# Kernel tuning notes

Measured on AMD Instinct MI355X. Metric: run time of the kernel, lower is better.

The kernel has to match this reference:

```python
import jax, jax.numpy as jnp
import numpy as np

B, S, D, H, L, FF, V, NB, G, C = 8, 1024, 256, 8, 2, 1024, 32000, 20000, 12, 4
DH = D // H


def _layer_norm(x, g, b, eps=1e-5):
    m = x.mean(-1, keepdims=True)
    v = ((x - m) ** 2).mean(-1, keepdims=True)
    return (x - m) / jnp.sqrt(v + eps) * g + b


def setup_inputs() -> dict:
    key = jax.random.key(0)
    ks = jax.random.split(key, 32)
    w = lambda k, shape, s=0.05: (jax.random.normal(k, shape, dtype=jnp.float32) * s)
    inp = {
        'input_ids': jax.random.randint(ks[0], (B, S), 0, V),
        'ngram_ids': jax.random.randint(ks[1], (V, G), 0, NB),
        'tfidf_scores': jax.random.uniform(ks[2], (V,), dtype=jnp.float32),
        'emb': jax.random.uniform(ks[3], (V, D), minval=-0.1, maxval=0.1, dtype=jnp.float32).at[0].set(0.0),  # padding_idx=0 row zeroed
        'pos_enc': jax.random.normal(ks[4], (1, S, D), dtype=jnp.float32) * 0.01,
        'bucket_emb': jax.random.uniform(ks[5], (NB, D), minval=-0.05, maxval=0.05, dtype=jnp.float32),
        'Wq': w(ks[6], (L, D, D)), 'bq': jnp.zeros((L, D)),
        'Wk': w(ks[7], (L, D, D)), 'bk': jnp.zeros((L, D)),
        'Wv': w(ks[8], (L, D, D)), 'bv': jnp.zeros((L, D)),
        'Wo': w(ks[9], (L, D, D)), 'bo': jnp.zeros((L, D)),
        'g1': jnp.ones((L, D)), 'be1': jnp.zeros((L, D)),
        'g2': jnp.ones((L, D)), 'be2': jnp.zeros((L, D)),
        'W1': w(ks[10], (L, D, FF)), 'b1': jnp.zeros((L, FF)),
        'W2': w(ks[11], (L, FF, D)), 'b2': jnp.zeros((L, D)),
        'alpha': jnp.full((L,), 0.1, dtype=jnp.float32),
        'gf': jnp.ones((D,)), 'bf': jnp.zeros((D,)),
        'Wc': jax.random.uniform(ks[12], (D, C), minval=-0.1, maxval=0.1, dtype=jnp.float32),
        'bc': jnp.zeros((C,)),
    }
    return inp


def reference(input_ids, ngram_ids, tfidf_scores, emb, pos_enc, bucket_emb,
              Wq, bq, Wk, bk, Wv, bv, Wo, bo, g1, be1, g2, be2,
              W1, b1, W2, b2, alpha, gf, bf, Wc, bc):
    pad_mask = input_ids == 0                      # (B,S) key padding mask
    x = emb[input_ids] + pos_enc[:, :S]            # (B,S,D)
    # char n-gram embedding: masked mean over n-gram buckets
    tok_ng = ngram_ids[jnp.clip(input_ids, 0, ngram_ids.shape[0] - 1)]   # (B,S,G)
    e_ng = bucket_emb[tok_ng]                       # (B,S,G,D)
    m = (tok_ng != 0)[..., None].astype(x.dtype)
    x = x + (e_ng * m).sum(axis=2) / jnp.clip(m.sum(axis=2), 1.0, None)
    # TF-IDF bias per key position
    bias_base = tfidf_scores[jnp.clip(input_ids, 0, tfidf_scores.shape[0] - 1)]  # (B,S)
    scale = DH ** -0.5
    for l in range(L):
        x2 = _layer_norm(x, g1[l], be1[l])
        Q = (x2 @ Wq[l] + bq[l]).reshape(B, S, H, DH).transpose(0, 2, 1, 3)
        K = (x2 @ Wk[l] + bk[l]).reshape(B, S, H, DH).transpose(0, 2, 1, 3)
        Vv = (x2 @ Wv[l] + bv[l]).reshape(B, S, H, DH).transpose(0, 2, 1, 3)
        scores = jnp.einsum('bhqd,bhkd->bhqk', Q, K) * scale
        scores = scores + (bias_base * alpha[l])[:, None, None, :]
        scores = jnp.where(pad_mask[:, None, None, :], -jnp.inf, scores)
        attn = jax.nn.softmax(scores, axis=-1)
        out = jnp.einsum('bhqk,bhkd->bhqd', attn, Vv).transpose(0, 2, 1, 3).reshape(B, S, D)
        x = x + (out @ Wo[l] + bo[l])
        x2 = _layer_norm(x, g2[l], be2[l])
        x = x + (jax.nn.relu(x2 @ W1[l] + b1[l]) @ W2[l] + b2[l])
    x = _layer_norm(x, gf, bf)
    return x[:, 0] @ Wc + bc                        # CLS pooling -> (B,4)
```

## Files before the change

kernel.cpp:

```cpp
#include <hip/hip_runtime.h>
#include <hip/hip_bf16.h>
#include <math.h>

#define TOK 8192
#define DIM 256
#define SEQ 1024
#define NH 8
#define FFD 1024
#define NL 2
#define VOCAB 32000
#define QKSTRIDE 2097152

typedef short bf16x8 __attribute__((ext_vector_type(8)));
typedef float f32x4 __attribute__((ext_vector_type(4)));

__device__ __forceinline__ ushort f2bf(float f) {
  union { float f; uint32_t u; } v; v.f = f;
  uint32_t r = v.u + 0x7FFFu + ((v.u >> 16) & 1u);
  return (ushort)(r >> 16);
}

__device__ __forceinline__ float bf2f(ushort u) {
  union { uint32_t u; float f; } v; v.u = (uint32_t)u << 16; return v.f;
}

__device__ __forceinline__ float exp2_n(float x) {
  float r; asm("v_exp_f32 %0, %1" : "=v"(r) : "v"(x)); return r;
}

__device__ __forceinline__ uint32_t cvtpk(float lo, float hi) {
  uint32_t r; asm("v_cvt_pk_bf16_f32 %0, %1, %2" : "=v"(r) : "v"(lo), "v"(hi));
  return r;
}

__device__ __forceinline__ void gload_lds16(const ushort* gp, ushort* lp) {
  __builtin_amdgcn_global_load_lds(
      (const __attribute__((address_space(1))) void*)gp,
      (__attribute__((address_space(3))) void*)lp, 16, 0, 0);
}

__global__ __launch_bounds__(256) void embed_ln_kernel(
    const int* __restrict__ ids, const int* __restrict__ ngram_ids,
    const float* __restrict__ tfidf, const float* __restrict__ emb,
    const float* __restrict__ pos, const float* __restrict__ bucket,
    const float* __restrict__ alpha, const float* __restrict__ g1,
    const float* __restrict__ be1,
    float* __restrict__ x, ushort* __restrict__ x2b, float* __restrict__ bm2)
{
  __shared__ int ngs[4][12];
  const int wave = threadIdx.x >> 6, lane = threadIdx.x & 63;
  const int t = blockIdx.x * 4 + wave;
  const int id = ids[t];
  int idc = id; if (idc < 0) idc = 0; if (idc > VOCAB-1) idc = VOCAB-1;
  if (lane < 12) ngs[wave][lane] = ngram_ids[idc*12 + lane];
  if (lane == 0) {
    const float tf = tfidf[idc];
    const bool msk = (id == 0);
    const float l2e = 1.4426950408889634f;
    bm2[t]       = msk ? -1e30f : tf * alpha[0] * l2e;
    bm2[TOK + t] = msk ? -1e30f : tf * alpha[1] * l2e;
  }
  __syncthreads();
  const int d0 = lane * 4;
  const int s = t & (SEQ - 1);
  float4 v = *reinterpret_cast<const float4*>(emb + (size_t)id*DIM + d0);
  const float4 p4 = *reinterpret_cast<const float4*>(pos + s*DIM + d0);
  v.x += p4.x; v.y += p4.y; v.z += p4.z; v.w += p4.w;
  float4 sum = {0.f, 0.f, 0.f, 0.f}; int cnt = 0;
  #pragma unroll
  for (int g = 0; g < 12; ++g) {
    const int ng = ngs[wave][g];
    if (ng != 0) {
      const float4 b4 = *reinterpret_cast<const float4*>(bucket + (size_t)ng*DIM + d0);
      sum.x += b4.x; sum.y += b4.y; sum.z += b4.z; sum.w += b4.w;
      cnt++;
    }
  }
  const float inv = 1.f / fmaxf((float)cnt, 1.0f);
  v.x += sum.x*inv; v.y += sum.y*inv; v.z += sum.z*inv; v.w += sum.w*inv;
  *reinterpret_cast<float4*>(x + (size_t)t*DIM + d0) = v;
  float sm = v.x + v.y + v.z + v.w;
  #pragma unroll
  for (int o = 32; o >= 1; o >>= 1) sm += __shfl_xor(sm, o);
  const float mean = sm * (1.f/256.f);
  const float dx0 = v.x-mean, dx1 = v.y-mean, dx2 = v.z-mean, dx3 = v.w-mean;
  float q = dx0*dx0 + dx1*dx1 + dx2*dx2 + dx3*dx3;
  #pragma unroll
  for (int o = 32; o >= 1; o >>= 1) q += __shfl_xor(q, o);
  const float rs = rsqrtf(q * (1.f/256.f) + 1e-5f);
  const float4 gv = *reinterpret_cast<const float4*>(g1 + d0);
  const float4 bv = *reinterpret_cast<const float4*>(be1 + d0);
  ushort4 o4;
  o4.x = f2bf(dx0*rs*gv.x + bv.x);
  o4.y = f2bf(dx1*rs*gv.y + bv.y);
  o4.z = f2bf(dx2*rs*gv.z + bv.z);
  o4.w = f2bf(dx3*rs*gv.w + bv.w);
  *reinterpret_cast<ushort4*>(x2b + (size_t)t*DIM + d0) = o4;
}

__global__ __launch_bounds__(256) void ln_bf16(
    const float* __restrict__ x, const float* __restrict__ g,
    const float* __restrict__ b, ushort* __restrict__ y)
{
  const int wave = threadIdx.x >> 6, lane = threadIdx.x & 63;
  const int row = blockIdx.x * 4 + wave;
  const float* xr = x + (size_t)row * DIM;
  float4 v = *reinterpret_cast<const float4*>(xr + lane*4);
  float s = v.x + v.y + v.z + v.w;
  #pragma unroll
  for (int o = 32; o >= 1; o >>= 1) s += __shfl_xor(s, o);
  const float mean = s * (1.f/256.f);
  const float dx0 = v.x-mean, dx1 = v.y-mean, dx2 = v.z-mean, dx3 = v.w-mean;
  float q = dx0*dx0 + dx1*dx1 + dx2*dx2 + dx3*dx3;
  #pragma unroll
  for (int o = 32; o >= 1; o >>= 1) q += __shfl_xor(q, o);
  const float rs = rsqrtf(q * (1.f/256.f) + 1e-5f);
  float4 gv = *reinterpret_cast<const float4*>(g + lane*4);
  float4 bv = *reinterpret_cast<const float4*>(b + lane*4);
  ushort4 o4;
  o4.x = f2bf(dx0*rs*gv.x + bv.x);
  o4.y = f2bf(dx1*rs*gv.y + bv.y);
  o4.z = f2bf(dx2*rs*gv.z + bv.z);
  o4.w = f2bf(dx3*rs*gv.w + bv.w);
  *reinterpret_cast<ushort4*>(y + (size_t)row*DIM + lane*4) = o4;
}

struct TDesc { const float* src; ushort* dst; int K; int N; };
struct TDescs { TDesc d[12]; };

__global__ __launch_bounds__(256) void transpose_conv(TDescs descs)
{
  const TDesc t = descs.d[blockIdx.z];
  const int k0 = blockIdx.x * 32, n0 = blockIdx.y * 32;
  if (k0 >= t.K || n0 >= t.N) return;
  __shared__ float tile[32][33];
  const int r = threadIdx.x >> 5, cc = threadIdx.x & 31;
  #pragma unroll
  for (int i = 0; i < 4; ++i)
    tile[r + i*8][cc] = t.src[(size_t)(k0 + r + i*8)*t.N + n0 + cc];
  __syncthreads();
  #pragma unroll
  for (int i = 0; i < 4; ++i)
    t.dst[(size_t)(n0 + r + i*8)*t.K + k0 + cc] = f2bf(tile[cc][r + i*8]);
}

template<int KDIM, int NDIM, int MODE>
__global__ __launch_bounds__(256) void gemm_mfma(
    const ushort* __restrict__ A, const ushort* __restrict__ Bw,
    const float* __restrict__ bias0, const float* __restrict__ bias1,
    const float* __restrict__ bias2, void* __restrict__ Cout,
    ushort* __restrict__ vtb)
{
  __shared__ ushort Al[3][64*32];
  __shared__ ushort Bl[3][128*32];
  const int bm = blockIdx.y * 64, bn = blockIdx.x * 128;
  const int tid = threadIdx.x, w = tid >> 6, lane = tid & 63;
  const int g = lane >> 4, c = lane & 15;
  const int lrow = lane >> 2, lc8 = (lane & 3) << 3;
  const f32x4 fzero = {0.f, 0.f, 0.f, 0.f};
  f32x4 acc[4][2];
  #pragma unroll
  for (int m = 0; m < 4; ++m) { acc[m][0] = fzero; acc[m][1] = fzero; }

#define STAGE(buf, k0)                                                         \
  {                                                                            \
    _Pragma("unroll")                                                          \
    for (int ch = w; ch < 12; ch += 4) {                                       \
      if (ch < 4)                                                              \
        gload_lds16(A + (size_t)(bm + ch*16 + lrow)*KDIM + (k0) + lc8,         \
                    &Al[buf][ch*512]);                                         \
      else                                                                     \
        gload_lds16(Bw + (size_t)(bn + (ch-4)*16 + lrow)*KDIM + (k0) + lc8,    \
                    &Bl[buf][(ch-4)*512]);                                     \
    }                                                                          \
  }

#define COMPUTE(buf)                                                           \
  {                                                                            \
    bf16x8 af[4], bfr[2];                                                      \
    _Pragma("unroll")                                                          \
    for (int m = 0; m < 4; ++m)                                                \
      af[m] = *(const bf16x8*)&Al[buf][(m*16 + c)*32 + g*8];                   \
    _Pragma("unroll")                                                          \
    for (int n = 0; n < 2; ++n)                                                \
      bfr[n] = *(const bf16x8*)&Bl[buf][(w*32 + n*16 + c)*32 + g*8];           \
    _Pragma("unroll")                                                          \
    for (int m = 0; m < 4; ++m)                                                \
      _Pragma("unroll")                                                        \
      for (int n = 0; n < 2; ++n)                                              \
        acc[m][n] = __builtin_amdgcn_mfma_f32_16x16x32_bf16(af[m], bfr[n], acc[m][n], 0, 0, 0); \
  }

  STAGE(0, 0);
  STAGE(1, 32);
  STAGE(2, 64);
  int buf = 0;
  for (int k0 = 0; k0 + 64 < KDIM; k0 += 32) {
    asm volatile("s_waitcnt vmcnt(6)" ::: "memory");
    __builtin_amdgcn_s_barrier();
    COMPUTE(buf);
    asm volatile("s_waitcnt lgkmcnt(0)" ::: "memory");
    __builtin_amdgcn_s_barrier();
    if (k0 + 96 < KDIM) STAGE(buf, k0 + 96);
    buf = (buf == 2) ? 0 : buf + 1;
  }
  asm volatile("s_waitcnt vmcnt(3)" ::: "memory");
  __builtin_amdgcn_s_barrier();
  COMPUTE(buf);
  buf = (buf == 2) ? 0 : buf + 1;
  asm volatile("s_waitcnt vmcnt(0)" ::: "memory");
  __builtin_amdgcn_s_barrier();
  COMPUTE(buf);
#undef STAGE
#undef COMPUTE

  #pragma unroll
  for (int m = 0; m < 4; ++m) {
    const int row0 = bm + m*16 + g*4;
    #pragma unroll
    for (int n = 0; n < 2; ++n) {
      const int col = bn + w*32 + n*16 + c;
      if (MODE == 1) {
        const float bb = bias0[col];
        #pragma unroll
        for (int r = 0; r < 4; ++r) {
          const float vv = fmaxf(acc[m][n][r] + bb, 0.f);
          const float other = __shfl_xor(vv, 1);
          if ((c & 1) == 0) {
            const uint32_t word = (uint32_t)f2bf(vv) | ((uint32_t)f2bf(other) << 16);
            *(uint32_t*)((ushort*)Cout + (size_t)(row0 + r)*NDIM + col) = word;
          }
        }
      } else if (MODE == 4) {
        const int b_ = row0 >> 10, s = row0 & (SEQ - 1);
        const int hd = col & 255;
        const int hh = hd >> 5, d = hd & 31;
        const float bb = (col < 256) ? bias0[hd] : bias1[hd];
        ushort* dst = ((col < 256) ? (ushort*)Cout : vtb)
                    + (((size_t)(b_*NH + hh)*SEQ + s) << 5) + d;
        #pragma unroll
        for (int r = 0; r < 4; ++r) {
          const float vv = acc[m][n][r] + bb;
          const float other = __shfl_xor(vv, 1);
          if ((c & 1) == 0) {
            const uint32_t word = (uint32_t)f2bf(vv) | ((uint32_t)f2bf(other) << 16);
            *(uint32_t*)(dst + (r << 5)) = word;
          }
        }
      } else {
        const int b_ = row0 >> 10, s = row0 & (SEQ - 1);
        if (col < 512) {
          const int hd = col & 255;
          const int hh = hd >> 5, d = hd & 31;
          const float bb = (col < 256) ? bias0[hd] : bias1[hd];
          ushort* dst = (ushort*)Cout + (col < 256 ? 0 : QKSTRIDE)
                      + (((size_t)(b_*NH + hh)*SEQ + s) << 5) + d;
          #pragma unroll
          for (int r = 0; r < 4; ++r) {
            const float vv = acc[m][n][r] + bb;
            const float other = __shfl_xor(vv, 1);
            if ((c & 1) == 0) {
              const uint32_t word = (uint32_t)f2bf(vv) | ((uint32_t)f2bf(other) << 16);
              *(uint32_t*)(dst + (r << 5)) = word;
            }
          }
        } else {
          const int hd = col - 512;
          const int hh = hd >> 5, d = hd & 31;
          const float bb = bias2[hd];
          const int sg = s >> 5, a = (s & 31) >> 2;
          const int pbase = (a & 3)*8 + (a >> 2)*4;
          ushort4 w4;
          w4.x = f2bf(acc[m][n][0] + bb);
          w4.y = f2bf(acc[m][n][1] + bb);
          w4.z = f2bf(acc[m][n][2] + bb);
          w4.w = f2bf(acc[m][n][3] + bb);
          *(ushort4*)(vtb + (((size_t)((b_*NH + hh)*32 + sg)*32 + d) << 5) + pbase) = w4;
        }
      }
    }
  }
}

template<int KDIM>
__global__ __launch_bounds__(256) void gemm64_acc(
    const ushort* __restrict__ A, const ushort* __restrict__ Bw,
    const float* __restrict__ bias, float* __restrict__ C)
{
  __shared__ ushort Al[3][64*32];
  __shared__ ushort Bl[3][64*32];
  const int bm = blockIdx.y * 64, bn = blockIdx.x * 64;
  const int tid = threadIdx.x, w = tid >> 6, lane = tid & 63;
  const int wm = w >> 1, wn = w & 1;
  const int g = lane >> 4, c = lane & 15;
  const int lrow = tid >> 2, lc8 = (tid & 3) << 3;
  const f32x4 fzero = {0.f, 0.f, 0.f, 0.f};
  f32x4 acc[2][2];
  acc[0][0] = fzero; acc[0][1] = fzero; acc[1][0] = fzero; acc[1][1] = fzero;

#define STAGE64(buf, k0)                                                       \
  {                                                                            \
    gload_lds16(A  + (size_t)(bm + lrow)*KDIM + (k0) + lc8,                    \
                &Al[buf][lrow*32 + lc8]);                                      \
    gload_lds16(Bw + (size_t)(bn + lrow)*KDIM + (k0) + lc8,                    \
                &Bl[buf][lrow*32 + lc8]);                                      \
  }

#define COMPUTE64(buf)                                                         \
  {                                                                            \
    bf16x8 af[2], bfr[2];                                                      \
    _Pragma("unroll")                                                          \
    for (int m = 0; m < 2; ++m)                                                \
      af[m] = *(const bf16x8*)&Al[buf][(wm*32 + m*16 + c)*32 + g*8];           \
    _Pragma("unroll")                                                          \
    for (int n = 0; n < 2; ++n)                                                \
      bfr[n] = *(const bf16x8*)&Bl[buf][(wn*32 + n*16 + c)*32 + g*8];          \
    _Pragma("unroll")                                                          \
    for (int m = 0; m < 2; ++m)                                                \
      _Pragma("unroll")                                                        \
      for (int n = 0; n < 2; ++n)                                              \
        acc[m][n] = __builtin_amdgcn_mfma_f32_16x16x32_bf16(af[m], bfr[n], acc[m][n], 0, 0, 0); \
  }

  STAGE64(0, 0);
  STAGE64(1, 32);
  STAGE64(2, 64);
  int buf = 0;
  for (int k0 = 0; k0 + 64 < KDIM; k0 += 32) {
    asm volatile("s_waitcnt vmcnt(4)" ::: "memory");
    __builtin_amdgcn_s_barrier();
    COMPUTE64(buf);
    asm volatile("s_waitcnt lgkmcnt(0)" ::: "memory");
    __builtin_amdgcn_s_barrier();
    if (k0 + 96 < KDIM) STAGE64(buf, k0 + 96);
    buf = (buf == 2) ? 0 : buf + 1;
  }
  asm volatile("s_waitcnt vmcnt(2)" ::: "memory");
  __builtin_amdgcn_s_barrier();
  COMPUTE64(buf);
  buf = (buf == 2) ? 0 : buf + 1;
  asm volatile("s_waitcnt vmcnt(0)" ::: "memory");
  __builtin_amdgcn_s_barrier();
  COMPUTE64(buf);
#undef STAGE64
#undef COMPUTE64

  #pragma unroll
  for (int m = 0; m < 2; ++m) {
    const int row0 = bm + wm*32 + m*16 + g*4;
    #pragma unroll
    for (int n = 0; n < 2; ++n) {
      const int col = bn + wn*32 + n*16 + c;
      const float bb = bias[col];
      #pragma unroll
      for (int r = 0; r < 4; ++r)
        C[(size_t)(row0 + r)*DIM + col] += acc[m][n][r] + bb;
    }
  }
}

__global__ __launch_bounds__(256) void attn_mfma(
    const ushort* __restrict__ qh, const ushort* __restrict__ kh,
    const ushort* __restrict__ vph, const float* __restrict__ bm2l,
    ushort* __restrict__ O)
{
  const int bid = blockIdx.x;
  const int lin = ((bid & 7) << 8) + (bid >> 3);
  const int tid = threadIdx.x, w = tid >> 6, lane = tid & 63;
  const int qw = lin & 31, h = (lin >> 5) & 7, b = lin >> 8;
  const int qb = qw << 5;
  const float scale2 = 0.17677669529663687f * 1.4426950408889634f;
  const int g = lane >> 4, c = lane & 15;
  const f32x4 fzero = {0.f, 0.f, 0.f, 0.f};
  const size_t bh = (size_t)(b*NH + h);

  const bf16x8 qf0 = *(const bf16x8*)(qh + ((bh*SEQ + qb + c)      << 5) + g*8);
  const bf16x8 qf1 = *(const bf16x8*)(qh + ((bh*SEQ + qb + 16 + c) << 5) + g*8);
  const ushort* kbase = kh  + ((bh*SEQ) << 5) + g*8;
  const ushort* vbase = vph + ((bh*SEQ) << 5) + g*8;
  const float*  bmb   = bm2l + b*SEQ;

  f32x4 oacc[2][2];
  oacc[0][0] = fzero; oacc[0][1] = fzero; oacc[1][0] = fzero; oacc[1][1] = fzero;
  float l0 = 0.f, l1 = 0.f;

  bf16x8 kfA[4], kfB[4];
  bf16x8 vfA[2][2], vfB[2][2];

#define LOADT(kt, kf, vf)                                                      \
  {                                                                            \
    _Pragma("unroll")                                                          \
    for (int ks = 0; ks < 4; ++ks)                                             \
      kf[ks] = *(const bf16x8*)(kbase + (((kt) + ks*16 + c) << 5));            \
    _Pragma("unroll")                                                          \
    for (int ds_ = 0; ds_ < 2; ++ds_)                                          \
      _Pragma("unroll")                                                        \
      for (int sg = 0; sg < 2; ++sg)                                           \
        vf[ds_][sg] = *(const bf16x8*)(vbase +                                 \
            (((((kt) >> 5) + sg)*32 + ds_*16 + c) << 5));                      \
  }

#define ATILE(kf, vf, kt)                                                      \
  {                                                                            \
    f32x4 sf0[4], sf1[4];                                                      \
    __builtin_amdgcn_s_setprio(1);                                             \
    _Pragma("unroll")                                                          \
    for (int ks = 0; ks < 4; ++ks)                                             \
      sf0[ks] = __builtin_amdgcn_mfma_f32_16x16x32_bf16(kf[ks], qf0, fzero, 0, 0, 0); \
    _Pragma("unroll")                                                          \
    for (int ks = 0; ks < 4; ++ks)                                             \
      sf1[ks] = __builtin_amdgcn_mfma_f32_16x16x32_bf16(kf[ks], qf1, fzero, 0, 0, 0); \
    __builtin_amdgcn_s_setprio(0);                                             \
    float e0[4][4], e1[4][4];                                                  \
    _Pragma("unroll")                                                          \
    for (int ks = 0; ks < 4; ++ks) {                                           \
      const f32x4 bb = *(const f32x4*)(bmb + (kt) + ks*16 + g*4);              \
      _Pragma("unroll")                                                        \
      for (int r = 0; r < 4; ++r) {                                            \
        e0[ks][r] = exp2_n(fmaf(sf0[ks][r], scale2, bb[r]));                   \
        e1[ks][r] = exp2_n(fmaf(sf1[ks][r], scale2, bb[r]));                   \
      }                                                                        \
    }                                                                          \
    float a0 = 0.f, a1 = 0.f, a2 = 0.f, a3 = 0.f;                              \
    _Pragma("unroll")                                                          \
    for (int r = 0; r < 4; ++r) {                                              \
      a0 += e0[0][r] + e0[1][r]; a1 += e0[2][r] + e0[3][r];                    \
      a2 += e1[0][r] + e1[1][r]; a3 += e1[2][r] + e1[3][r];                    \
    }                                                                          \
    l0 += a0 + a1; l1 += a2 + a3;                                              \
    union { bf16x8 v; uint32_t u[4]; } p00, p01, p10, p11;                     \
    p00.u[0] = cvtpk(e0[0][0], e0[0][1]); p00.u[1] = cvtpk(e0[0][2], e0[0][3]);\
    p00.u[2] = cvtpk(e0[1][0], e0[1][1]); p00.u[3] = cvtpk(e0[1][2], e0[1][3]);\
    p01.u[0] = cvtpk(e0[2][0], e0[2][1]); p01.u[1] = cvtpk(e0[2][2], e0[2][3]);\
    p01.u[2] = cvtpk(e0[3][0], e0[3][1]); p01.u[3] = cvtpk(e0[3][2], e0[3][3]);\
    p10.u[0] = cvtpk(e1[0][0], e1[0][1]); p10.u[1] = cvtpk(e1[0][2], e1[0][3]);\
    p10.u[2] = cvtpk(e1[1][0], e1[1][1]); p10.u[3] = cvtpk(e1[1][2], e1[1][3]);\
    p11.u[0] = cvtpk(e1[2][0], e1[2][1]); p11.u[1] = cvtpk(e1[2][2], e1[2][3]);\
    p11.u[2] = cvtpk(e1[3][0], e1[3][1]); p11.u[3] = cvtpk(e1[3][2], e1[3][3]);\
    __builtin_amdgcn_s_setprio(1);                                             \
    oacc[0][0] = __builtin_amdgcn_mfma_f32_16x16x32_bf16(vf[0][0], p00.v, oacc[0][0], 0, 0, 0); \
    oacc[0][1] = __builtin_amdgcn_mfma_f32_16x16x32_bf16(vf[1][0], p00.v, oacc[0][1], 0, 0, 0); \
    oacc[1][0] = __builtin_amdgcn_mfma_f32_16x16x32_bf16(vf[0][0], p10.v, oacc[1][0], 0, 0, 0); \
    oacc[1][1] = __builtin_amdgcn_mfma_f32_16x16x32_bf16(vf[1][0], p10.v, oacc[1][1], 0, 0, 0); \
    oacc[0][0] = __builtin_amdgcn_mfma_f32_16x16x32_bf16(vf[0][1], p01.v, oacc[0][0], 0, 0, 0); \
    oacc[0][1] = __builtin_amdgcn_mfma_f32_16x16x32_bf16(vf[1][1], p01.v, oacc[0][1], 0, 0, 0); \
    oacc[1][0] = __builtin_amdgcn_mfma_f32_16x16x32_bf16(vf[0][1], p11.v, oacc[1][0], 0, 0, 0); \
    oacc[1][1] = __builtin_amdgcn_mfma_f32_16x16x32_bf16(vf[1][1], p11.v, oacc[1][1], 0, 0, 0); \
    __builtin_amdgcn_s_setprio(0);                                             \
  }

  const int kt0 = w << 8;
  LOADT(kt0, kfA, vfA);
  LOADT(kt0 + 64, kfB, vfB);
  ATILE(kfA, vfA, kt0);
  LOADT(kt0 + 128, kfA, vfA);
  ATILE(kfB, vfB, kt0 + 64);
  LOADT(kt0 + 192, kfB, vfB);
  ATILE(kfA, vfA, kt0 + 128);
  ATILE(kfB, vfB, kt0 + 192);
#undef LOADT
#undef ATILE

  __shared__ float Lo[4][64][19];
  #pragma unroll
  for (int q = 0; q < 2; ++q)
    #pragma unroll
    for (int ds_ = 0; ds_ < 2; ++ds_)
      #pragma unroll
      for (int i = 0; i < 4; ++i)
        Lo[w][lane][q*8 + ds_*4 + i] = oacc[q][ds_][i];
  Lo[w][lane][16] = l0;
  Lo[w][lane][17] = l1;
  __syncthreads();
  if (w < 2) {
    const int q = w;
    float o[8] = {0.f,0.f,0.f,0.f,0.f,0.f,0.f,0.f};
    float ls = 0.f;
    #pragma unroll
    for (int ww = 0; ww < 4; ++ww) {
      ls += Lo[ww][lane][16 + q];
      #pragma unroll
      for (int i = 0; i < 8; ++i) o[i] += Lo[ww][lane][q*8 + i];
    }
    ls += __shfl_xor(ls, 16);
    ls += __shfl_xor(ls, 32);
    const float inv = 1.f / ls;
    ushort* orow = O + (size_t)(b*SEQ + qb + q*16 + c)*DIM + h*32 + g*4;
    const uint32_t w0 = (uint32_t)f2bf(o[0]*inv) | ((uint32_t)f2bf(o[1]*inv) << 16);
    const uint32_t w1 = (uint32_t)f2bf(o[2]*inv) | ((uint32_t)f2bf(o[3]*inv) << 16);
    const uint32_t w2 = (uint32_t)f2bf(o[4]*inv) | ((uint32_t)f2bf(o[5]*inv) << 16);
    const uint32_t w3 = (uint32_t)f2bf(o[6]*inv) | ((uint32_t)f2bf(o[7]*inv) << 16);
    *(uint32_t*)(orow)      = w0;
    *(uint32_t*)(orow + 2)  = w1;
    *(uint32_t*)(orow + 16) = w2;
    *(uint32_t*)(orow + 18) = w3;
  }
}

__global__ __launch_bounds__(256) void decode512(
    const ushort* __restrict__ x2b, const ushort* __restrict__ Wq1,
    const float* __restrict__ bq1, const ushort* __restrict__ kh,
    const ushort* __restrict__ vh, const float* __restrict__ bm2l,
    float* __restrict__ P)
{
  const int lin = blockIdx.x;
  const int ks = lin & 3, bh = lin >> 2;
  const int b = bh >> 3, h = bh & 7;
  const int tid = threadIdx.x;
  const float scale2 = 0.17677669529663687f * 1.4426950408889634f;
  __shared__ float xrow[256];
  __shared__ float qv[32];
  xrow[tid] = bf2f(x2b[(size_t)(b*SEQ)*DIM + tid]);
  __syncthreads();
  if (tid < 32) {
    const ushort* wrow = Wq1 + (size_t)(h*32 + tid)*DIM;
    float acc = bq1[h*32 + tid];
    #pragma unroll
    for (int k8 = 0; k8 < 32; ++k8) {
      const bf16x8 wv = *(const bf16x8*)(wrow + k8*8);
      #pragma unroll
      for (int j = 0; j < 8; ++j)
        acc = fmaf(bf2f((ushort)wv[j]), xrow[k8*8 + j], acc);
    }
    qv[tid] = acc;
  }
  __syncthreads();
  const int key = ks*256 + tid;
  const ushort* kr = kh + (((size_t)bh*SEQ + key) << 5);
  float dot = 0.f;
  #pragma unroll
  for (int i = 0; i < 4; ++i) {
    const bf16x8 kv8 = *(const bf16x8*)(kr + i*8);
    #pragma unroll
    for (int j = 0; j < 8; ++j)
      dot = fmaf(bf2f((ushort)kv8[j]), qv[i*8 + j], dot);
  }
  const float e = exp2_n(fmaf(dot, scale2, bm2l[b*SEQ + key]));
  const ushort* vr = vh + (((size_t)bh*SEQ + key) << 5);
  __shared__ float red[256][33];
  #pragma unroll
  for (int i = 0; i < 4; ++i) {
    const bf16x8 vv8 = *(const bf16x8*)(vr + i*8);
    #pragma unroll
    for (int j = 0; j < 8; ++j)
      red[tid][i*8 + j] = e * bf2f((ushort)vv8[j]);
  }
  red[tid][32] = e;
  __syncthreads();
  for (int s = 128; s >= 1; s >>= 1) {
    for (int i = tid; i < s*33; i += 256) {
      const int r = i / 33, d = i - r*33;
      red[r][d] += red[r + s][d];
    }
    __syncthreads();
  }
  if (tid < 33) P[((size_t)bh*4 + ks)*33 + tid] = red[0][tid];
}

__global__ __launch_bounds__(256) void wo_part(
    const float* __restrict__ P, const ushort* __restrict__ WoT1,
    const float* __restrict__ bo1, float* __restrict__ wo_out)
{
  const int cc = blockIdx.x, tid = threadIdx.x;
  __shared__ float orow[8][256];
  {
    const int b = tid >> 5, d32 = tid & 31;
    #pragma unroll
    for (int h = 0; h < 8; ++h) {
      const float* pp = P + ((size_t)(b*8 + h)*4)*33;
      float ov = 0.f, l = 0.f;
      #pragma unroll
      for (int ks = 0; ks < 4; ++ks) { ov += pp[ks*33 + d32]; l += pp[ks*33 + 32]; }
      orow[b][h*32 + d32] = ov / l;
    }
  }
  __syncthreads();
  const int w = tid >> 6, lane = tid & 63;
  const int col = cc*4 + w;
  const ushort* wrow = WoT1 + (size_t)col*DIM + lane*4;
  float wk[4];
  #pragma unroll
  for (int j = 0; j < 4; ++j) wk[j] = bf2f(wrow[j]);
  #pragma unroll
  for (int b = 0; b < 8; ++b) {
    float p = 0.f;
    #pragma unroll
    for (int j = 0; j < 4; ++j) p = fmaf(wk[j], orow[b][lane*4 + j], p);
    #pragma unroll
    for (int off = 32; off >= 1; off >>= 1) p += __shfl_xor(p, off);
    if (lane == 0) wo_out[b*DIM + col] = p + bo1[col];
  }
}

__global__ __launch_bounds__(256) void ff1_part(
    const float* __restrict__ x, const float* __restrict__ wo_out,
    const float* __restrict__ g21, const float* __restrict__ be21,
    const ushort* __restrict__ W1T1, const float* __restrict__ b11,
    float* __restrict__ mid)
{
  const int cc = blockIdx.x, tid = threadIdx.x;
  const int wave = tid >> 6, lane = tid & 63;
  __shared__ float trow[8][256];
  #pragma unroll
  for (int b = 0; b < 8; ++b)
    trow[b][tid] = x[(size_t)(b*SEQ)*DIM + tid] + wo_out[b*DIM + tid];
  __syncthreads();
  #pragma unroll
  for (int bb_ = 0; bb_ < 2; ++bb_) {
    const int b = wave + bb_*4;
    float4 vv = *(float4*)&trow[b][lane*4];
    float sm = vv.x + vv.y + vv.z + vv.w;
    #pragma unroll
    for (int o = 32; o >= 1; o >>= 1) sm += __shfl_xor(sm, o);
    const float mean = sm * (1.f/256.f);
    const float dx0 = vv.x-mean, dx1 = vv.y-mean, dx2 = vv.z-mean, dx3 = vv.w-mean;
    float q = dx0*dx0 + dx1*dx1 + dx2*dx2 + dx3*dx3;
    #pragma unroll
    for (int o = 32; o >= 1; o >>= 1) q += __shfl_xor(q, o);
    const float rs = rsqrtf(q * (1.f/256.f) + 1e-5f);
    const float4 gv = *(const float4*)(g21 + lane*4);
    const float4 bv = *(const float4*)(be21 + lane*4);
    float4 nv;
    nv.x = dx0*rs*gv.x + bv.x;
    nv.y = dx1*rs*gv.y + bv.y;
    nv.z = dx2*rs*gv.z + bv.z;
    nv.w = dx3*rs*gv.w + bv.w;
    *(float4*)&trow[b][lane*4] = nv;
  }
  __syncthreads();
  const int dotid = tid >> 1;
  const int col = cc*16 + (dotid & 15);
  const int b = dotid >> 4;
  const int kh_ = (tid & 1) * 128;
  const ushort* wrow = W1T1 + (size_t)col*DIM + kh_;
  float acc = 0.f;
  #pragma unroll
  for (int k8 = 0; k8 < 16; ++k8) {
    const bf16x8 wv = *(const bf16x8*)(wrow + k8*8);
    #pragma unroll
    for (int j = 0; j < 8; ++j)
      acc = fmaf(bf2f((ushort)wv[j]), trow[b][kh_ + k8*8 + j], acc);
  }
  acc += __shfl_xor(acc, 1);
  if ((tid & 1) == 0) mid[b*FFD + col] = fmaxf(acc + b11[col], 0.f);
}

__global__ __launch_bounds__(256) void ff2_part(
    const float* __restrict__ mid, const ushort* __restrict__ W2T1,
    const float* __restrict__ b21, const float* __restrict__ x,
    const float* __restrict__ wo_out, float* __restrict__ y2)
{
  const int cc = blockIdx.x, tid = threadIdx.x;
  __shared__ float mrow[8][1024];
  #pragma unroll
  for (int i = 0; i < 32; ++i) {
    const int idx = i*256 + tid;
    mrow[idx >> 10][idx & 1023] = mid[idx];
  }
  __syncthreads();
  const int dotid = tid >> 3;
  const int col = cc*4 + (dotid & 3);
  const int b = dotid >> 2;
  const int seg = (tid & 7) * 128;
  const ushort* wrow = W2T1 + (size_t)col*FFD + seg;
  float acc = 0.f;
  #pragma unroll
  for (int k8 = 0; k8 < 16; ++k8) {
    const bf16x8 wv = *(const bf16x8*)(wrow + k8*8);
    #pragma unroll
    for (int j = 0; j < 8; ++j)
      acc = fmaf(bf2f((ushort)wv[j]), mrow[b][seg + k8*8 + j], acc);
  }
  acc += __shfl_xor(acc, 1);
  acc += __shfl_xor(acc, 2);
  acc += __shfl_xor(acc, 4);
  if ((tid & 7) == 0)
    y2[b*DIM + col] = x[(size_t)(b*SEQ)*DIM + col] + wo_out[b*DIM + col]
                    + acc + b21[col];
}

__global__ __launch_bounds__(256) void cls2(
    const float* __restrict__ y2, const float* __restrict__ gf,
    const float* __restrict__ bfb, const float* __restrict__ Wc,
    const float* __restrict__ bc, float* __restrict__ out)
{
  const int b = blockIdx.x, tid = threadIdx.x;
  const int wave = tid >> 6, lane = tid & 63;
  const float v = y2[b*DIM + tid];
  __shared__ float redm[4], redv[4], redc[4][4];
  float s = v;
  #pragma unroll
  for (int o = 32; o >= 1; o >>= 1) s += __shfl_xor(s, o);
  if (lane == 0) redm[wave] = s;
  __syncthreads();
  const float mean = (redm[0]+redm[1]+redm[2]+redm[3]) * (1.f/256.f);
  const float dv = v - mean;
  float q = dv * dv;
  #pragma unroll
  for (int o = 32; o >= 1; o >>= 1) q += __shfl_xor(q, o);
  if (lane == 0) redv[wave] = q;
  __syncthreads();
  const float var = (redv[0]+redv[1]+redv[2]+redv[3]) * (1.f/256.f);
  const float rs = rsqrtf(var + 1e-5f);
  const float yn = dv*rs*gf[tid] + bfb[tid];
  float pc[4];
  #pragma unroll
  for (int cc = 0; cc < 4; ++cc) pc[cc] = yn * Wc[tid*4 + cc];
  #pragma unroll
  for (int cc = 0; cc < 4; ++cc) {
    #pragma unroll
    for (int o = 32; o >= 1; o >>= 1) pc[cc] += __shfl_xor(pc[cc], o);
  }
  if (lane == 0) {
    #pragma unroll
    for (int cc = 0; cc < 4; ++cc) redc[wave][cc] = pc[cc];
  }
  __syncthreads();
  if (tid < 4)
    out[b*4 + tid] = redc[0][tid] + redc[1][tid] + redc[2][tid] + redc[3][tid] + bc[tid];
}

extern "C" void kernel_launch(void* const* d_in, const int* in_sizes, int n_in,
                              void* d_out, int out_size, void* d_ws, size_t ws_size,
                              hipStream_t stream)
{
  const int*   ids    = (const int*)d_in[0];
  const int*   ngrams = (const int*)d_in[1];
  const float* tfidf  = (const float*)d_in[2];
  const float* emb    = (const float*)d_in[3];
  const float* pos    = (const float*)d_in[4];
  const float* bucket = (const float*)d_in[5];
  const float* Wq = (const float*)d_in[6];  const float* bq = (const float*)d_in[7];
  const float* Wk = (const float*)d_in[8];  const float* bk = (const float*)d_in[9];
  const float* Wv = (const float*)d_in[10]; const float* bv = (const float*)d_in[11];
  const float* Wo = (const float*)d_in[12]; const float* bo = (const float*)d_in[13];
  const float* g1 = (const float*)d_in[14]; const float* be1= (const float*)d_in[15];
  const float* g2 = (const float*)d_in[16]; const float* be2= (const float*)d_in[17];
  const float* W1 = (const float*)d_in[18]; const float* b1 = (const float*)d_in[19];
  const float* W2 = (const float*)d_in[20]; const float* b2 = (const float*)d_in[21];
  const float* alpha = (const float*)d_in[22];
  const float* gf = (const float*)d_in[23]; const float* bf = (const float*)d_in[24];
  const float* Wc = (const float*)d_in[25]; const float* bc = (const float*)d_in[26];

  uint8_t* base = (uint8_t*)d_ws;
  float*  x      = (float*)  base;
  ushort* x2b    = (ushort*)(base + 8388608);
  ushort* qkh    = (ushort*)(base + 12582912);
  ushort* vtb    = (ushort*)(base + 20971520);
  ushort* attb   = (ushort*)(base + 25165824);
  ushort* midb   = (ushort*)(base + 29360128);
  float*  bm2    = (float*) (base + 46137344);
  ushort* WqkvT  = (ushort*)(base + 46202880);
  ushort* WoT    = (ushort*)(base + 46989312);
  ushort* W1T    = (ushort*)(base + 47251456);
  ushort* W2T    = (ushort*)(base + 48300032);

  float* P       = (float*)(base + 25165824);
  float* wo_out  = (float*)(base + 25165824 + 65536);
  float* midf    = (float*)(base + 25165824 + 90112);
  float* y2      = (float*)(base + 25165824 + 122880);

  TDescs td;
  for (int l = 0; l < NL; ++l) {
    td.d[6*l+0] = { Wq + (size_t)l*DIM*DIM, WqkvT + (size_t)l*768*DIM +   0*DIM, DIM, DIM };
    td.d[6*l+1] = { Wk + (size_t)l*DIM*DIM, WqkvT + (size_t)l*768*DIM + 256*DIM, DIM, DIM };
    td.d[6*l+2] = { Wv + (size_t)l*DIM*DIM, WqkvT + (size_t)l*768*DIM + 512*DIM, DIM, DIM };
    td.d[6*l+3] = { Wo + (size_t)l*DIM*DIM, WoT  + (size_t)l*DIM*DIM,  DIM, DIM };
    td.d[6*l+4] = { W1 + (size_t)l*DIM*FFD, W1T  + (size_t)l*FFD*DIM,  DIM, FFD };
    td.d[6*l+5] = { W2 + (size_t)l*FFD*DIM, W2T  + (size_t)l*DIM*FFD,  FFD, DIM };
  }
  transpose_conv<<<dim3(32, 32, 12), 256, 0, stream>>>(td);

  embed_ln_kernel<<<TOK/4, 256, 0, stream>>>(
      ids, ngrams, tfidf, emb, pos, bucket, alpha, g1, be1, x, x2b, bm2);

  const dim3 gqkv(6, TOK/64), gkv(4, TOK/64), gff1(8, TOK/64), g64(4, TOK/64);

  gemm_mfma<256, 768, 3><<<gqkv, 256, 0, stream>>>(
      x2b, WqkvT, bq, bk, bv, qkh, vtb);
  attn_mfma<<<2048, 256, 0, stream>>>(qkh, qkh + QKSTRIDE, vtb, bm2, attb);
  gemm64_acc<256><<<g64, 256, 0, stream>>>(attb, WoT, bo, x);
  ln_bf16<<<TOK/4, 256, 0, stream>>>(x, g2, be2, x2b);
  gemm_mfma<256, 1024, 1><<<gff1, 256, 0, stream>>>(
      x2b, W1T, b1, nullptr, nullptr, midb, nullptr);
  gemm64_acc<1024><<<g64, 256, 0, stream>>>(midb, W2T, b2, x);

  ln_bf16<<<TOK/4, 256, 0, stream>>>(x, g1 + DIM, be1 + DIM, x2b);
  gemm_mfma<256, 512, 4><<<gkv, 256, 0, stream>>>(
      x2b, WqkvT + (size_t)768*DIM + 256*DIM, bk + DIM, bv + DIM, nullptr,
      qkh + QKSTRIDE, vtb);
  decode512<<<256, 256, 0, stream>>>(
      x2b, WqkvT + (size_t)768*DIM, bq + DIM,
      qkh + QKSTRIDE, vtb, bm2 + TOK, P);
  wo_part<<<64, 256, 0, stream>>>(P, WoT + DIM*DIM, bo + DIM, wo_out);
  ff1_part<<<64, 256, 0, stream>>>(x, wo_out, g2 + DIM, be2 + DIM,
                                   W1T + FFD*DIM, b1 + FFD, midf);
  ff2_part<<<64, 256, 0, stream>>>(midf, W2T + DIM*FFD, b2 + DIM, x, wo_out, y2);
  cls2<<<8, 256, 0, stream>>>(y2, gf, bf, Wc, bc, (float*)d_out);
}
```

Baseline: 143.7 us.

## Split attention warps across query and key groups, halving block count

The attention kernel now gives each block 64 queries instead of 32, with its four warps arranged as two query groups by two key halves of 512 keys each, in place of four key quarters over the same 32 queries. The grid shrinks from 2048 to 1024 blocks, and the cross-warp reduction now sums two partials per query group and writes both 16-row sub-tiles. This halves the block-level overhead and the reduction work per output row, at the cost of longer per-warp key loops and fewer blocks to spread across compute units.

```diff
diff --git a/kernel.cpp b/kernel.cpp
--- a/kernel.cpp
+++ b/kernel.cpp
@@ -365,10 +365,11 @@
     ushort* __restrict__ O)
 {
   const int bid = blockIdx.x;
-  const int lin = ((bid & 7) << 8) + (bid >> 3);
+  const int lin = ((bid & 7) << 7) + (bid >> 3);
   const int tid = threadIdx.x, w = tid >> 6, lane = tid & 63;
-  const int qw = lin & 31, h = (lin >> 5) & 7, b = lin >> 8;
-  const int qb = qw << 5;
+  const int q64 = lin & 15, h = (lin >> 4) & 7, b = lin >> 7;
+  const int qg = w >> 1, kg = w & 1;
+  const int qb = (q64 << 6) + (qg << 5);
   const float scale2 = 0.17677669529663687f * 1.4426950408889634f;
   const int g = lane >> 4, c = lane & 15;
   const f32x4 fzero = {0.f, 0.f, 0.f, 0.f};
@@ -449,15 +450,14 @@
     __builtin_amdgcn_s_setprio(0);                                             \
   }
 
-  const int kt0 = w << 8;
+  const int kt0 = kg << 9;
   LOADT(kt0, kfA, vfA);
-  LOADT(kt0 + 64, kfB, vfB);
-  ATILE(kfA, vfA, kt0);
-  LOADT(kt0 + 128, kfA, vfA);
-  ATILE(kfB, vfB, kt0 + 64);
-  LOADT(kt0 + 192, kfB, vfB);
-  ATILE(kfA, vfA, kt0 + 128);
-  ATILE(kfB, vfB, kt0 + 192);
+  for (int kt = kt0; kt < kt0 + 512; kt += 128) {
+    LOADT(kt + 64, kfB, vfB);
+    ATILE(kfA, vfA, kt);
+    if (kt + 128 < kt0 + 512) LOADT(kt + 128, kfA, vfA);
+    ATILE(kfB, vfB, kt + 64);
+  }
 #undef LOADT
 #undef ATILE
 
@@ -473,27 +473,29 @@
   Lo[w][lane][17] = l1;
   __syncthreads();
   if (w < 2) {
-    const int q = w;
-    float o[8] = {0.f,0.f,0.f,0.f,0.f,0.f,0.f,0.f};
-    float ls = 0.f;
-    #pragma unroll
-    for (int ww = 0; ww < 4; ++ww) {
-      ls += Lo[ww][lane][16 + q];
+    const int qgv = w;
+    const int w0i = qgv*2, w1i = qgv*2 + 1;
+    #pragma unroll
+    for (int q = 0; q < 2; ++q) {
+      float o[8];
       #pragma unroll
-      for (int i = 0; i < 8; ++i) o[i] += Lo[ww][lane][q*8 + i];
+      for (int i = 0; i < 8; ++i)
+        o[i] = Lo[w0i][lane][q*8 + i] + Lo[w1i][lane][q*8 + i];
+      float ls = Lo[w0i][lane][16 + q] + Lo[w1i][lane][16 + q];
+      ls += __shfl_xor(ls, 16);
+      ls += __shfl_xor(ls, 32);
+      const float inv = 1.f / ls;
+      const int row = (q64 << 6) + (qgv << 5) + q*16 + c;
+      ushort* orow = O + (size_t)(b*SEQ + row)*DIM + h*32 + g*4;
+      const uint32_t w0 = (uint32_t)f2bf(o[0]*inv) | ((uint32_t)f2bf(o[1]*inv) << 16);
+      const uint32_t w1 = (uint32_t)f2bf(o[2]*inv) | ((uint32_t)f2bf(o[3]*inv) << 16);
+      const uint32_t w2 = (uint32_t)f2bf(o[4]*inv) | ((uint32_t)f2bf(o[5]*inv) << 16);
+      const uint32_t w3 = (uint32_t)f2bf(o[6]*inv) | ((uint32_t)f2bf(o[7]*inv) << 16);
+      *(uint32_t*)(orow)      = w0;
+      *(uint32_t*)(orow + 2)  = w1;
+      *(uint32_t*)(orow + 16) = w2;
+      *(uint32_t*)(orow + 18) = w3;
     }
-    ls += __shfl_xor(ls, 16);
-    ls += __shfl_xor(ls, 32);
-    const float inv = 1.f / ls;
-    ushort* orow = O + (size_t)(b*SEQ + qb + q*16 + c)*DIM + h*32 + g*4;
-    const uint32_t w0 = (uint32_t)f2bf(o[0]*inv) | ((uint32_t)f2bf(o[1]*inv) << 16);
-    const uint32_t w1 = (uint32_t)f2bf(o[2]*inv) | ((uint32_t)f2bf(o[3]*inv) << 16);
-    const uint32_t w2 = (uint32_t)f2bf(o[4]*inv) | ((uint32_t)f2bf(o[5]*inv) << 16);
-    const uint32_t w3 = (uint32_t)f2bf(o[6]*inv) | ((uint32_t)f2bf(o[7]*inv) << 16);
-    *(uint32_t*)(orow)      = w0;
-    *(uint32_t*)(orow + 2)  = w1;
-    *(uint32_t*)(orow + 16) = w2;
-    *(uint32_t*)(orow + 18) = w3;
   }
 }
 
@@ -778,7 +780,7 @@
 
   gemm_mfma<256, 768, 3><<<gqkv, 256, 0, stream>>>(
       x2b, WqkvT, bq, bk, bv, qkh, vtb);
-  attn_mfma<<<2048, 256, 0, stream>>>(qkh, qkh + QKSTRIDE, vtb, bm2, attb);
+  attn_mfma<<<1024, 256, 0, stream>>>(qkh, qkh + QKSTRIDE, vtb, bm2, attb);
   gemm64_acc<256><<<g64, 256, 0, stream>>>(attb, WoT, bo, x);
   ln_bf16<<<TOK/4, 256, 0, stream>>>(x, g2, be2, x2b);
   gemm_mfma<256, 1024, 1><<<gff1, 256, 0, stream>>>(
```

Result: faster. 140.3 us (-2.4%).
